# Kernel optimization log

Measured on AMD Instinct MI355X. Metric: run time of the kernel, lower is better.

The kernel has to match this reference:

```python
import jax, jax.numpy as jnp
import numpy as np

N_NODES = 100000
N_EDGES = 3200000
IN_C, HID_C, OUT_C = 5, 128, 64


def setup_inputs() -> dict:
    key = jax.random.key(0)
    k_x, k_e, k_w1, k_b1, k_w2, k_b2 = jax.random.split(key, 6)
    x = jax.random.normal(k_x, (N_NODES, IN_C), dtype=jnp.float32)
    edge_index = jax.random.randint(k_e, (2, N_EDGES), 0, N_NODES, dtype=jnp.int32)
    # GCNConv learned params (glorot weights, zero-ish bias)
    W1 = jax.random.normal(k_w1, (IN_C, HID_C), dtype=jnp.float32) * (1.0 / np.sqrt(IN_C))
    b1 = jax.random.normal(k_b1, (HID_C,), dtype=jnp.float32) * 0.01
    W2 = jax.random.normal(k_w2, (HID_C, OUT_C), dtype=jnp.float32) * (1.0 / np.sqrt(HID_C))
    b2 = jax.random.normal(k_b2, (OUT_C,), dtype=jnp.float32) * 0.01
    return {"x": x, "edge_index": edge_index, "W1": W1, "b1": b1, "W2": W2, "b2": b2}


def _gcn_conv(x, src, dst, deg_inv_sqrt, W, b):
    """One GCNConv (PyG defaults: self-loops already in src/dst, symmetric norm, bias)."""
    h = x @ W                                   # [N, C_out]
    norm = deg_inv_sqrt[src] * deg_inv_sqrt[dst]  # [E+N]
    msg = h[src] * norm[:, None]                # gather + scale
    out = jax.ops.segment_sum(msg, dst, num_segments=x.shape[0])  # scatter-add
    return out + b


def reference(x, edge_index, W1, b1, W2, b2):
    n = x.shape[0]
    loop = jnp.arange(n, dtype=edge_index.dtype)
    src = jnp.concatenate([edge_index[0], loop])  # self-loops appended
    dst = jnp.concatenate([edge_index[1], loop])
    deg = jax.ops.segment_sum(jnp.ones_like(src, dtype=x.dtype), dst, num_segments=n)
    deg_inv_sqrt = jnp.where(deg > 0, jax.lax.rsqrt(deg), 0.0)
    h = _gcn_conv(x, src, dst, deg_inv_sqrt, W1, b1)
    z = _gcn_conv(h, src, dst, deg_inv_sqrt, W2, b2)
    return z
```

## Files before the change

kernel.cpp:

```cpp
#include <hip/hip_runtime.h>

#define IN_C  5
#define HID_C 128
#define OUT_C 64

#define KB   256
#define NBP  512
#define CAP  10240
#define TILE 8192
#define BTH  512
#define EPT  (TILE / BTH)
#define GNODES 64


__global__ void k_init(int* __restrict__ gcursor) {
    gcursor[threadIdx.x] = threadIdx.x * CAP;
}

__global__ __launch_bounds__(BTH) void k_bin(const int* __restrict__ src,
                                             const int* __restrict__ dstp,
                                             int* __restrict__ gcursor,
                                             int* __restrict__ binned, int e) {
    __shared__ int lhist[NBP];
    __shared__ int lfill[NBP];
    __shared__ int lgpos[NBP];
    int tid = threadIdx.x;
    int tbeg = blockIdx.x * TILE;
    for (int j = tid; j < NBP; j += BTH) { lhist[j] = 0; lfill[j] = 0; }
    __syncthreads();
    int pk[EPT], bk[EPT];
    #pragma unroll
    for (int q = 0; q < EPT; ++q) {
        int idx = tbeg + q * BTH + tid;
        if (idx < e) {
            int s = src[idx], d = dstp[idx];
            pk[q] = ((d & 255) << 24) | s;
            bk[q] = ((unsigned)d) >> 8;
            atomicAdd(&lhist[bk[q]], 1);
        } else bk[q] = -1;
    }
    __syncthreads();
    int hv = lhist[tid];
    if (hv > 0) lgpos[tid] = atomicAdd(&gcursor[tid], hv);
    __syncthreads();
    #pragma unroll
    for (int q = 0; q < EPT; ++q) {
        if (bk[q] >= 0) {
            int pos = lgpos[bk[q]] + atomicAdd(&lfill[bk[q]], 1);
            binned[pos] = pk[q];
        }
    }
}

__global__ __launch_bounds__(BTH) void k_build(int* __restrict__ binned,
                                               const int* __restrict__ gcursor,
                                               const float* __restrict__ x,
                                               int* __restrict__ pstart,
                                               int* __restrict__ pend,
                                               float* __restrict__ xs, int n) {
    __shared__ int cnt[KB];
    __shared__ int wt[4];
    __shared__ int wte[4];
    __shared__ int stage[CAP];
    int tid = threadIdx.x;
    int lane = tid & 63, w = tid >> 6;
    int bkt = blockIdx.x;
    int beg = bkt * CAP;
    int tot = gcursor[bkt] - beg;
    if (tid < KB) cnt[tid] = 0;
    __syncthreads();
    for (int j0 = tid << 2; j0 < tot; j0 += BTH * 4) {
        int4 vv = *(const int4*)(binned + beg + j0);
        atomicAdd(&cnt[((unsigned)vv.x) >> 24], 1);
        if (j0 + 1 < tot) atomicAdd(&cnt[((unsigned)vv.y) >> 24], 1);
        if (j0 + 2 < tot) atomicAdd(&cnt[((unsigned)vv.z) >> 24], 1);
        if (j0 + 3 < tot) atomicAdd(&cnt[((unsigned)vv.w) >> 24], 1);
    }
    __syncthreads();
    int deg = (tid < KB) ? cnt[tid] : 0;
    int v = deg;
    #pragma unroll
    for (int m = 1; m < 64; m <<= 1) { int u = __shfl_up(v, m); if (lane >= m) v += u; }
    if (tid < KB && lane == 63) wt[w] = v;
    __syncthreads();
    if (tid == 0) {
        int s = 0;
        #pragma unroll
        for (int k = 0; k < 4; ++k) { wte[k] = s; s += wt[k]; }
    }
    __syncthreads();
    if (tid < KB) {
        int rel = wte[w] + v - deg;
        int node = bkt * KB + tid;
        pstart[node] = beg + rel;
        pend[node] = beg + rel + deg;
        cnt[tid] = rel;
        float d = rsqrtf(1.0f + (float)deg);
        float4 q0 = {0, 0, 0, 0}, q1 = {0, 0, 0, 0};
        if (node < n) {
            q0.x = x[node * IN_C + 0] * d;
            q0.y = x[node * IN_C + 1] * d;
            q0.z = x[node * IN_C + 2] * d;
            q0.w = x[node * IN_C + 3] * d;
            q1.x = x[node * IN_C + 4] * d;
            q1.y = d;
        }
        ((float4*)(xs + (size_t)node * 8))[0] = q0;
        ((float4*)(xs + (size_t)node * 8))[1] = q1;
    }
    __syncthreads();
    for (int j0 = tid << 2; j0 < tot; j0 += BTH * 4) {
        int4 vv = *(const int4*)(binned + beg + j0);
        {
            int slot = atomicAdd(&cnt[((unsigned)vv.x) >> 24], 1);
            stage[slot] = vv.x & 0xFFFFFF;
        }
        if (j0 + 1 < tot) {
            int slot = atomicAdd(&cnt[((unsigned)vv.y) >> 24], 1);
            stage[slot] = vv.y & 0xFFFFFF;
        }
        if (j0 + 2 < tot) {
            int slot = atomicAdd(&cnt[((unsigned)vv.z) >> 24], 1);
            stage[slot] = vv.z & 0xFFFFFF;
        }
        if (j0 + 3 < tot) {
            int slot = atomicAdd(&cnt[((unsigned)vv.w) >> 24], 1);
            stage[slot] = vv.w & 0xFFFFFF;
        }
    }
    __syncthreads();
    for (int j = tid; j < tot; j += BTH)
        binned[beg + j] = stage[j];
}

__global__ __launch_bounds__(BTH) void k_gath0(const int* __restrict__ srclist,
                                               const int* __restrict__ pstart,
                                               const int* __restrict__ pend,
                                               const float* __restrict__ feat,
                                               float* __restrict__ outf,
                                               float* __restrict__ tout, int n) {
    int tid = threadIdx.x;
    int node = blockIdx.x * GNODES + (tid >> 3);
    int sub = tid & 7;
    if (node >= n) return;
    int ps = pstart[node], pe = pend[node];
    float a0 = 0, a1 = 0, a2 = 0, a3 = 0, a4 = 0, a5 = 0;
    int j = ps + sub;
    for (; j + 8 < pe; j += 16) {
        int sA = srclist[j], sB = srclist[j + 8];
        const float4* qA = (const float4*)(feat + (size_t)sA * 8);
        const float4* qB = (const float4*)(feat + (size_t)sB * 8);
        float4 rA0 = qA[0], rA1 = qA[1];
        float4 rB0 = qB[0], rB1 = qB[1];
        a0 += rA0.x + rB0.x;
        a1 += rA0.y + rB0.y;
        a2 += rA0.z + rB0.z;
        a3 += rA0.w + rB0.w;
        a4 += rA1.x + rB1.x;
        a5 += rA1.y + rB1.y;
    }
    for (; j < pe; j += 8) {
        int sA = srclist[j];
        const float4* qA = (const float4*)(feat + (size_t)sA * 8);
        float4 rA0 = qA[0], rA1 = qA[1];
        a0 += rA0.x; a1 += rA0.y; a2 += rA0.z; a3 += rA0.w; a4 += rA1.x;
        a5 += rA1.y;
    }
    #pragma unroll
    for (int m = 1; m < 8; m <<= 1) {
        a0 += __shfl_xor(a0, m);
        a1 += __shfl_xor(a1, m);
        a2 += __shfl_xor(a2, m);
        a3 += __shfl_xor(a3, m);
        a4 += __shfl_xor(a4, m);
        a5 += __shfl_xor(a5, m);
    }
    if (sub == 0) {
        const float4* psr = (const float4*)(feat + (size_t)node * 8);
        float4 s0 = psr[0], s1 = psr[1];
        float d = s1.y;
        a0 += s0.x; a1 += s0.y; a2 += s0.z; a3 += s0.w; a4 += s1.x;
        a5 += s1.y;
        float d2 = d * d;
        float4 o0, o1;
        o0.x = d2 * a0; o0.y = d2 * a1; o0.z = d2 * a2; o0.w = d2 * a3;
        o1.x = d2 * a4;
        o1.y = d;
        o1.z = 0.0f; o1.w = 0.0f;
        tout[node] = d * a5;
        ((float4*)(outf + (size_t)node * 8))[0] = o0;
        ((float4*)(outf + (size_t)node * 8))[1] = o1;
    }
}

__global__ __launch_bounds__(BTH) void k_gout(const int* __restrict__ srclist,
                                              const int* __restrict__ pstart,
                                              const int* __restrict__ pend,
                                              const float* __restrict__ feat,
                                              const float* __restrict__ t,
                                              const float* __restrict__ W1,
                                              const float* __restrict__ b1,
                                              const float* __restrict__ W2,
                                              const float* __restrict__ b2,
                                              float* __restrict__ out, int n) {
    __shared__ float snode[GNODES * 8];
    __shared__ float sW[IN_C * OUT_C + 2 * OUT_C];
    int tid = threadIdx.x;
    if (tid < IN_C * OUT_C) {
        int k = tid >> 6, c = tid & 63;
        float acc = 0.0f;
        for (int m = 0; m < HID_C; ++m)
            acc += W1[k * HID_C + m] * W2[m * OUT_C + c];
        sW[tid] = acc;
    } else if (tid < IN_C * OUT_C + OUT_C) {
        int c = tid - IN_C * OUT_C;
        float acc = 0.0f;
        for (int m = 0; m < HID_C; ++m)
            acc += b1[m] * W2[m * OUT_C + c];
        sW[tid] = acc;
    } else if (tid < IN_C * OUT_C + 2 * OUT_C) {
        sW[tid] = b2[tid - IN_C * OUT_C - OUT_C];
    }
    int node = blockIdx.x * GNODES + (tid >> 3);
    int sub = tid & 7;
    bool act = (node < n);
    float a0 = 0, a1 = 0, a2 = 0, a3 = 0, a4 = 0;
    if (act) {
        int ps = pstart[node], pe = pend[node];
        int j = ps + sub;
        for (; j + 8 < pe; j += 16) {
            int sA = srclist[j], sB = srclist[j + 8];
            const float4* qA = (const float4*)(feat + (size_t)sA * 8);
            const float4* qB = (const float4*)(feat + (size_t)sB * 8);
            float4 rA0 = qA[0], rA1 = qA[1];
            float4 rB0 = qB[0], rB1 = qB[1];
            a0 += rA0.x + rB0.x;
            a1 += rA0.y + rB0.y;
            a2 += rA0.z + rB0.z;
            a3 += rA0.w + rB0.w;
            a4 += rA1.x + rB1.x;
        }
        for (; j < pe; j += 8) {
            int sA = srclist[j];
            const float4* qA = (const float4*)(feat + (size_t)sA * 8);
            float4 rA0 = qA[0], rA1 = qA[1];
            a0 += rA0.x; a1 += rA0.y; a2 += rA0.z; a3 += rA0.w; a4 += rA1.x;
        }
    }
    #pragma unroll
    for (int m = 1; m < 8; m <<= 1) {
        a0 += __shfl_xor(a0, m);
        a1 += __shfl_xor(a1, m);
        a2 += __shfl_xor(a2, m);
        a3 += __shfl_xor(a3, m);
        a4 += __shfl_xor(a4, m);
    }
    if (act && sub == 0) {
        const float4* psr = (const float4*)(feat + (size_t)node * 8);
        float4 s0 = psr[0], s1 = psr[1];
        float d = s1.y;
        a0 += s0.x; a1 += s0.y; a2 += s0.z; a3 += s0.w; a4 += s1.x;
        float* sn = snode + (tid >> 3) * 8;
        sn[0] = d * a0; sn[1] = d * a1; sn[2] = d * a2;
        sn[3] = d * a3; sn[4] = d * a4; sn[5] = t[node];
    }
    __syncthreads();
    int base = blockIdx.x * GNODES;
    for (int u = tid; u < GNODES * 16; u += BTH) {
        int ln = u >> 4, q = u & 15;
        int i = base + ln;
        if (i >= n) continue;
        const float* a = snode + ln * 8;
        float ti = a[5];
        float4 acc = ((const float4*)(sW + IN_C * OUT_C + OUT_C))[q];
        float4 bq  = ((const float4*)(sW + IN_C * OUT_C))[q];
        acc.x += ti * bq.x; acc.y += ti * bq.y;
        acc.z += ti * bq.z; acc.w += ti * bq.w;
        #pragma unroll
        for (int k = 0; k < IN_C; ++k) {
            float ak = a[k];
            float4 wk = ((const float4*)(sW + k * OUT_C))[q];
            acc.x += ak * wk.x; acc.y += ak * wk.y;
            acc.z += ak * wk.z; acc.w += ak * wk.w;
        }
        ((float4*)out)[(size_t)i * 16 + q] = acc;
    }
}

extern "C" void kernel_launch(void* const* d_in, const int* in_sizes, int n_in,
                              void* d_out, int out_size, void* d_ws, size_t ws_size,
                              hipStream_t stream) {
    const float* x   = (const float*)d_in[0];
    const int*   ei  = (const int*)d_in[1];
    const float* W1  = (const float*)d_in[2];
    const float* b1  = (const float*)d_in[3];
    const float* W2  = (const float*)d_in[4];
    const float* b2  = (const float*)d_in[5];
    float* out = (float*)d_out;

    const int n = in_sizes[0] / IN_C;
    const int e = in_sizes[1] / 2;
    const int* src = ei;
    const int* dst = ei + e;
    const int NB = (n + KB - 1) / KB;
    const int NKB = NB * KB;

    int*   gcursor = (int*)d_ws;
    int*   binned  = gcursor + 512;
    int*   pstart  = binned + (size_t)NBP * CAP;
    int*   pend    = pstart + NKB;
    float* xs      = (float*)(pend + NKB);
    float* p1      = xs + (size_t)8 * NKB;
    float* t       = p1 + (size_t)8 * NKB;

    const int gB = (e + TILE - 1) / TILE;
    const int gG = (n + GNODES - 1) / GNODES;

    k_init  <<<1, 512, 0, stream>>>(gcursor);
    k_bin   <<<gB, BTH, 0, stream>>>(src, dst, gcursor, binned, e);
    k_build <<<NB, BTH, 0, stream>>>(binned, gcursor, x, pstart, pend, xs, n);
    k_gath0 <<<gG, BTH, 0, stream>>>(binned, pstart, pend, xs, p1, t, n);
    k_gout  <<<gG, BTH, 0, stream>>>(binned, pstart, pend, p1, t,
                                     W1, b1, W2, b2, out, n);
}
```

Before: 188.4 us.

## Halve bin tile, cache bucket edges in registers, pack offsets, unroll gathers

Several independent tweaks. The binning tile is halved to 4096 edges so more blocks launch. In k_build, each thread keeps the bucket entries it loaded in a five-slot int4 register array, so the scatter pass reuses them instead of reading global memory a second time. The pstart/pend arrays are packed into one int2 array so each node needs a single 8-byte load, and the gather loops are unrolled to four independent neighbour fetches per iteration to keep more loads in flight. The trade-offs are higher register pressure and more bucket-cursor atomics from the smaller tiles; the five-slot array also only covers CAP entries per bucket.

```diff
diff --git a/kernel.cpp b/kernel.cpp
--- a/kernel.cpp
+++ b/kernel.cpp
@@ -7,7 +7,7 @@
 #define KB   256
 #define NBP  512
 #define CAP  10240
-#define TILE 8192
+#define TILE 4096
 #define BTH  512
 #define EPT  (TILE / BTH)
 #define GNODES 64
@@ -55,8 +55,7 @@
 __global__ __launch_bounds__(BTH) void k_build(int* __restrict__ binned,
                                                const int* __restrict__ gcursor,
                                                const float* __restrict__ x,
-                                               int* __restrict__ pstart,
-                                               int* __restrict__ pend,
+                                               int2* __restrict__ pse,
                                                float* __restrict__ xs, int n) {
     __shared__ int cnt[KB];
     __shared__ int wt[4];
@@ -69,12 +68,17 @@
     int tot = gcursor[bkt] - beg;
     if (tid < KB) cnt[tid] = 0;
     __syncthreads();
-    for (int j0 = tid << 2; j0 < tot; j0 += BTH * 4) {
-        int4 vv = *(const int4*)(binned + beg + j0);
-        atomicAdd(&cnt[((unsigned)vv.x) >> 24], 1);
-        if (j0 + 1 < tot) atomicAdd(&cnt[((unsigned)vv.y) >> 24], 1);
-        if (j0 + 2 < tot) atomicAdd(&cnt[((unsigned)vv.z) >> 24], 1);
-        if (j0 + 3 < tot) atomicAdd(&cnt[((unsigned)vv.w) >> 24], 1);
+    int4 r[5];
+    #pragma unroll
+    for (int it = 0; it < 5; ++it) {
+        int j0 = (tid << 2) + it * (BTH * 4);
+        if (j0 < tot) {
+            r[it] = *(const int4*)(binned + beg + j0);
+            atomicAdd(&cnt[((unsigned)r[it].x) >> 24], 1);
+            if (j0 + 1 < tot) atomicAdd(&cnt[((unsigned)r[it].y) >> 24], 1);
+            if (j0 + 2 < tot) atomicAdd(&cnt[((unsigned)r[it].z) >> 24], 1);
+            if (j0 + 3 < tot) atomicAdd(&cnt[((unsigned)r[it].w) >> 24], 1);
+        }
     }
     __syncthreads();
     int deg = (tid < KB) ? cnt[tid] : 0;
@@ -92,8 +96,7 @@
     if (tid < KB) {
         int rel = wte[w] + v - deg;
         int node = bkt * KB + tid;
-        pstart[node] = beg + rel;
-        pend[node] = beg + rel + deg;
+        pse[node] = make_int2(beg + rel, beg + rel + deg);
         cnt[tid] = rel;
         float d = rsqrtf(1.0f + (float)deg);
         float4 q0 = {0, 0, 0, 0}, q1 = {0, 0, 0, 0};
@@ -109,23 +112,26 @@
         ((float4*)(xs + (size_t)node * 8))[1] = q1;
     }
     __syncthreads();
-    for (int j0 = tid << 2; j0 < tot; j0 += BTH * 4) {
-        int4 vv = *(const int4*)(binned + beg + j0);
-        {
-            int slot = atomicAdd(&cnt[((unsigned)vv.x) >> 24], 1);
-            stage[slot] = vv.x & 0xFFFFFF;
-        }
-        if (j0 + 1 < tot) {
-            int slot = atomicAdd(&cnt[((unsigned)vv.y) >> 24], 1);
-            stage[slot] = vv.y & 0xFFFFFF;
-        }
-        if (j0 + 2 < tot) {
-            int slot = atomicAdd(&cnt[((unsigned)vv.z) >> 24], 1);
-            stage[slot] = vv.z & 0xFFFFFF;
-        }
-        if (j0 + 3 < tot) {
-            int slot = atomicAdd(&cnt[((unsigned)vv.w) >> 24], 1);
-            stage[slot] = vv.w & 0xFFFFFF;
+    #pragma unroll
+    for (int it = 0; it < 5; ++it) {
+        int j0 = (tid << 2) + it * (BTH * 4);
+        if (j0 < tot) {
+            {
+                int slot = atomicAdd(&cnt[((unsigned)r[it].x) >> 24], 1);
+                stage[slot] = r[it].x & 0xFFFFFF;
+            }
+            if (j0 + 1 < tot) {
+                int slot = atomicAdd(&cnt[((unsigned)r[it].y) >> 24], 1);
+                stage[slot] = r[it].y & 0xFFFFFF;
+            }
+            if (j0 + 2 < tot) {
+                int slot = atomicAdd(&cnt[((unsigned)r[it].z) >> 24], 1);
+                stage[slot] = r[it].z & 0xFFFFFF;
+            }
+            if (j0 + 3 < tot) {
+                int slot = atomicAdd(&cnt[((unsigned)r[it].w) >> 24], 1);
+                stage[slot] = r[it].w & 0xFFFFFF;
+            }
         }
     }
     __syncthreads();
@@ -134,8 +140,7 @@
 }
 
 __global__ __launch_bounds__(BTH) void k_gath0(const int* __restrict__ srclist,
-                                               const int* __restrict__ pstart,
-                                               const int* __restrict__ pend,
+                                               const int2* __restrict__ pse,
                                                const float* __restrict__ feat,
                                                float* __restrict__ outf,
                                                float* __restrict__ tout, int n) {
@@ -143,21 +148,27 @@
     int node = blockIdx.x * GNODES + (tid >> 3);
     int sub = tid & 7;
     if (node >= n) return;
-    int ps = pstart[node], pe = pend[node];
+    int2 pp = pse[node];
+    int ps = pp.x, pe = pp.y;
     float a0 = 0, a1 = 0, a2 = 0, a3 = 0, a4 = 0, a5 = 0;
     int j = ps + sub;
-    for (; j + 8 < pe; j += 16) {
-        int sA = srclist[j], sB = srclist[j + 8];
-        const float4* qA = (const float4*)(feat + (size_t)sA * 8);
-        const float4* qB = (const float4*)(feat + (size_t)sB * 8);
-        float4 rA0 = qA[0], rA1 = qA[1];
-        float4 rB0 = qB[0], rB1 = qB[1];
-        a0 += rA0.x + rB0.x;
-        a1 += rA0.y + rB0.y;
-        a2 += rA0.z + rB0.z;
-        a3 += rA0.w + rB0.w;
-        a4 += rA1.x + rB1.x;
-        a5 += rA1.y + rB1.y;
+    for (; j + 24 < pe; j += 32) {
+        int s0 = srclist[j],      s1 = srclist[j + 8];
+        int s2 = srclist[j + 16], s3 = srclist[j + 24];
+        const float4* q0 = (const float4*)(feat + (size_t)s0 * 8);
+        const float4* q1 = (const float4*)(feat + (size_t)s1 * 8);
+        const float4* q2 = (const float4*)(feat + (size_t)s2 * 8);
+        const float4* q3 = (const float4*)(feat + (size_t)s3 * 8);
+        float4 rA0 = q0[0], rA1 = q0[1];
+        float4 rB0 = q1[0], rB1 = q1[1];
+        float4 rC0 = q2[0], rC1 = q2[1];
+        float4 rD0 = q3[0], rD1 = q3[1];
+        a0 += (rA0.x + rB0.x) + (rC0.x + rD0.x);
+        a1 += (rA0.y + rB0.y) + (rC0.y + rD0.y);
+        a2 += (rA0.z + rB0.z) + (rC0.z + rD0.z);
+        a3 += (rA0.w + rB0.w) + (rC0.w + rD0.w);
+        a4 += (rA1.x + rB1.x) + (rC1.x + rD1.x);
+        a5 += (rA1.y + rB1.y) + (rC1.y + rD1.y);
     }
     for (; j < pe; j += 8) {
         int sA = srclist[j];
@@ -194,8 +205,7 @@
 }
 
 __global__ __launch_bounds__(BTH) void k_gout(const int* __restrict__ srclist,
-                                              const int* __restrict__ pstart,
-                                              const int* __restrict__ pend,
+                                              const int2* __restrict__ pse,
                                               const float* __restrict__ feat,
                                               const float* __restrict__ t,
                                               const float* __restrict__ W1,
@@ -226,19 +236,25 @@
     bool act = (node < n);
     float a0 = 0, a1 = 0, a2 = 0, a3 = 0, a4 = 0;
     if (act) {
-        int ps = pstart[node], pe = pend[node];
+        int2 pp = pse[node];
+        int ps = pp.x, pe = pp.y;
         int j = ps + sub;
-        for (; j + 8 < pe; j += 16) {
-            int sA = srclist[j], sB = srclist[j + 8];
-            const float4* qA = (const float4*)(feat + (size_t)sA * 8);
-            const float4* qB = (const float4*)(feat + (size_t)sB * 8);
-            float4 rA0 = qA[0], rA1 = qA[1];
-            float4 rB0 = qB[0], rB1 = qB[1];
-            a0 += rA0.x + rB0.x;
-            a1 += rA0.y + rB0.y;
-            a2 += rA0.z + rB0.z;
-            a3 += rA0.w + rB0.w;
-            a4 += rA1.x + rB1.x;
+        for (; j + 24 < pe; j += 32) {
+            int s0 = srclist[j],      s1 = srclist[j + 8];
+            int s2 = srclist[j + 16], s3 = srclist[j + 24];
+            const float4* q0 = (const float4*)(feat + (size_t)s0 * 8);
+            const float4* q1 = (const float4*)(feat + (size_t)s1 * 8);
+            const float4* q2 = (const float4*)(feat + (size_t)s2 * 8);
+            const float4* q3 = (const float4*)(feat + (size_t)s3 * 8);
+            float4 rA0 = q0[0], rA1 = q0[1];
+            float4 rB0 = q1[0], rB1 = q1[1];
+            float4 rC0 = q2[0], rC1 = q2[1];
+            float4 rD0 = q3[0], rD1 = q3[1];
+            a0 += (rA0.x + rB0.x) + (rC0.x + rD0.x);
+            a1 += (rA0.y + rB0.y) + (rC0.y + rD0.y);
+            a2 += (rA0.z + rB0.z) + (rC0.z + rD0.z);
+            a3 += (rA0.w + rB0.w) + (rC0.w + rD0.w);
+            a4 += (rA1.x + rB1.x) + (rC1.x + rD1.x);
         }
         for (; j < pe; j += 8) {
             int sA = srclist[j];
@@ -307,9 +323,8 @@
 
     int*   gcursor = (int*)d_ws;
     int*   binned  = gcursor + 512;
-    int*   pstart  = binned + (size_t)NBP * CAP;
-    int*   pend    = pstart + NKB;
-    float* xs      = (float*)(pend + NKB);
+    int2*  pse     = (int2*)(binned + (size_t)NBP * CAP);
+    float* xs      = (float*)(pse + NKB);
     float* p1      = xs + (size_t)8 * NKB;
     float* t       = p1 + (size_t)8 * NKB;
 
@@ -318,8 +333,8 @@
 
     k_init  <<<1, 512, 0, stream>>>(gcursor);
     k_bin   <<<gB, BTH, 0, stream>>>(src, dst, gcursor, binned, e);
-    k_build <<<NB, BTH, 0, stream>>>(binned, gcursor, x, pstart, pend, xs, n);
-    k_gath0 <<<gG, BTH, 0, stream>>>(binned, pstart, pend, xs, p1, t, n);
-    k_gout  <<<gG, BTH, 0, stream>>>(binned, pstart, pend, p1, t,
+    k_build <<<NB, BTH, 0, stream>>>(binned, gcursor, x, pse, xs, n);
+    k_gath0 <<<gG, BTH, 0, stream>>>(binned, pse, xs, p1, t, n);
+    k_gout  <<<gG, BTH, 0, stream>>>(binned, pse, p1, t,
                                      W1, b1, W2, b2, out, n);
 }
```

Measured after the change: 190.4 us. About the same (+1.1%).
